# Optimization experiments

Measured on AMD Instinct MI355X. Metric: run time of the kernel, lower is better.

## Reference

```python
import jax, jax.numpy as jnp
import numpy as np

D_MODEL = 1024
H = 16
D_K = D_MODEL // H


def setup_inputs() -> dict:
    key = jax.random.key(0)
    ks = jax.random.split(key, 9)
    B, S = 4, 2048
    s = 1.0 / np.sqrt(D_MODEL)
    return {
        "query": jax.random.normal(ks[0], (B, S, D_MODEL), jnp.float32),
        "key_": jax.random.normal(ks[1], (B, S, D_MODEL), jnp.float32),
        "value": jax.random.normal(ks[2], (B, S, D_MODEL), jnp.float32),
        "Wq": jax.random.normal(ks[3], (D_MODEL, D_MODEL), jnp.float32) * s,
        "bq": jnp.zeros((D_MODEL,), jnp.float32),
        "Wk": jax.random.normal(ks[4], (D_MODEL, D_MODEL), jnp.float32) * s,
        "bk": jnp.zeros((D_MODEL,), jnp.float32),
        "Wv": jax.random.normal(ks[5], (D_MODEL, D_MODEL), jnp.float32) * s,
        "bv": jnp.zeros((D_MODEL,), jnp.float32),
    }


def reference(query, key_, value, Wq, bq, Wk, bk, Wv, bv):
    B, S, _ = query.shape
    # separate Q/K/V projections (torch Linear: x @ W.T + b)
    q = (query @ Wq.T + bq).reshape(B, S, H, D_K).transpose(0, 2, 1, 3)  # [B,H,S,Dk]
    k = (key_ @ Wk.T + bk).reshape(B, S, H, D_K).transpose(0, 2, 1, 3)
    v = (value @ Wv.T + bv).reshape(B, S, H, D_K).transpose(0, 2, 1, 3)
    # naive scaled dot-product attention (full [B,H,S,S] scores)
    scores = jnp.einsum("bhqd,bhkd->bhqk", q, k) / jnp.sqrt(jnp.float32(D_K))
    attn = jax.nn.softmax(scores, axis=-1)
    out = jnp.einsum("bhqk,bhkd->bhqd", attn, v)  # [B,H,S,Dk]
    # merge heads; NOTE: original forward never applies self.wo
    return out.transpose(0, 2, 1, 3).reshape(B, S, D_MODEL)
```

## Files before the change

kernel.cpp:

```cpp
#include <hip/hip_runtime.h>
#include <math.h>

#define DEVI __device__ __forceinline__

typedef short bf16x8 __attribute__((ext_vector_type(8)));
typedef float f32x4 __attribute__((ext_vector_type(4)));
typedef float f32x16 __attribute__((ext_vector_type(16)));
typedef unsigned short u16x8 __attribute__((ext_vector_type(8)));
typedef unsigned short u16x4 __attribute__((ext_vector_type(4)));
typedef unsigned int u32x2 __attribute__((ext_vector_type(2)));
typedef int i32x4 __attribute__((ext_vector_type(4)));

static constexpr int S_LEN = 2048;
static constexpr int DMODEL = 1024;
static constexpr int NH = 16;
static constexpr int DK = 64;

DEVI unsigned short f2bf(float f) {
  unsigned int u = __builtin_bit_cast(unsigned int, f);
  u = u + 0x7fffu + ((u >> 16) & 1u);
  return (unsigned short)(u >> 16);
}
DEVI unsigned cvtpk(float lo, float hi) {
  unsigned d;
  asm("v_cvt_pk_bf16_f32 %0, %1, %2" : "=v"(d) : "v"(lo), "v"(hi));
  return d;
}
DEVI float bitf(unsigned u) { return __builtin_bit_cast(float, u); }
DEVI unsigned bitu(float f) { return __builtin_bit_cast(unsigned, f); }

#if __has_builtin(__builtin_amdgcn_exp2f)
DEVI float fexp2(float x) { return __builtin_amdgcn_exp2f(x); }
#else
DEVI float fexp2(float x) { return __expf(x * 0.69314718055994531f); }
#endif

typedef __attribute__((address_space(3))) unsigned int lds_u32;
typedef __attribute__((address_space(1))) const unsigned int glb_u32;

DEVI void gload16(const void* g, void* lds) {
  __builtin_amdgcn_global_load_lds((glb_u32*)reinterpret_cast<uintptr_t>(g),
                                   (lds_u32*)reinterpret_cast<uintptr_t>(lds),
                                   16, 0, 0);
}

__global__ __launch_bounds__(256) void cvt_w3(const float* __restrict__ w0,
                                              const float* __restrict__ w1,
                                              const float* __restrict__ w2,
                                              unsigned short* __restrict__ out) {
  const int i = blockIdx.x * 256 + threadIdx.x;
  const int z = i >> 17, j = i & 131071;
  const float* in = (z == 0) ? w0 : (z == 1) ? w1 : w2;
  const float4* p = (const float4*)in + (size_t)j * 2;
  float4 a = p[0], b = p[1];
  u16x8 o;
  o[0] = f2bf(a.x); o[1] = f2bf(a.y); o[2] = f2bf(a.z); o[3] = f2bf(a.w);
  o[4] = f2bf(b.x); o[5] = f2bf(b.y); o[6] = f2bf(b.z); o[7] = f2bf(b.w);
  *((u16x8*)(out + (size_t)z * 1048576) + j) = o;
}

__global__ __launch_bounds__(256) void proj_all(const float* __restrict__ Aq,
                                                const float* __restrict__ Ak,
                                                const float* __restrict__ Av,
                                                const unsigned short* __restrict__ Wb,
                                                const float* __restrict__ bq,
                                                const float* __restrict__ bk,
                                                const float* __restrict__ bv,
                                                unsigned short* __restrict__ Qh,
                                                unsigned short* __restrict__ Kh,
                                                unsigned short* __restrict__ Vt,
                                                float qscale) {
  const int z = blockIdx.z;
  const float* A = (z == 0) ? Aq : (z == 1) ? Ak : Av;
  const unsigned short* W = Wb + (size_t)z * 1048576;
  const float* bias = (z == 0) ? bq : (z == 1) ? bk : bv;
  unsigned short* C = (z == 0) ? Qh : (z == 1) ? Kh : Vt;
  const float scale = (z == 0) ? qscale : 1.0f;
  const bool VT = (z == 2);

  __shared__ unsigned short As[2][128 * 32];
  __shared__ unsigned short Bs[2][128 * 32];
  const int m0 = blockIdx.x * 128, n0 = blockIdx.y * 128;
  const int tid = threadIdx.x, wid = tid >> 6, lane = tid & 63;
  const int l15 = lane & 15, lg = lane >> 4;
  const int mb = (wid >> 1) * 64, nb = (wid & 1) * 64;

  const int arow = wid * 32 + (lane >> 3);
  const int acolb = (lane & 7) * 16;

  f32x4 acc[4][4] = {};
  float4 a4[4];

  auto LOADA = [&](int kk) {
#pragma unroll
    for (int i = 0; i < 4; ++i)
      a4[i] = *(const float4*)((const char*)A + (size_t)(m0 + arow + i * 8) * 4096 +
                               kk * 128 + acolb);
  };
  auto GLOADW = [&](int b, int kk) {
#pragma unroll
    for (int i = 0; i < 2; ++i) {
      const int jb = (wid * 2 + i) * 1024;
      const int o = jb + lane * 16;
      gload16((const char*)W + (size_t)(n0 + (o >> 6)) * 2048 + kk * 64 + (o & 63),
              (char*)&Bs[b][0] + jb);
    }
  };
  auto WRITEA = [&](int b) {
#pragma unroll
    for (int i = 0; i < 4; ++i) {
      u32x2 wv;
      wv[0] = cvtpk(a4[i].x, a4[i].y);
      wv[1] = cvtpk(a4[i].z, a4[i].w);
      *(u32x2*)((char*)&As[b][0] + (arow + i * 8) * 64 + (lane & 7) * 8) = wv;
    }
  };

  LOADA(0);
  GLOADW(0, 0);
  asm volatile("s_waitcnt vmcnt(0)" ::: "memory");
  WRITEA(0);
  __syncthreads();

  int buf = 0;
  for (int kk = 0; kk < 32; ++kk) {
    if (kk < 31) {
      LOADA(kk + 1);
      GLOADW(buf ^ 1, kk + 1);
    }

    bf16x8 af[4], bfr[4];
#pragma unroll
    for (int ms = 0; ms < 4; ++ms)
      af[ms] = *(const bf16x8*)&As[buf][(mb + ms * 16 + l15) * 32 + lg * 8];
#pragma unroll
    for (int ns = 0; ns < 4; ++ns)
      bfr[ns] = *(const bf16x8*)&Bs[buf][(nb + ns * 16 + l15) * 32 + lg * 8];
#pragma unroll
    for (int ms = 0; ms < 4; ++ms)
#pragma unroll
      for (int ns = 0; ns < 4; ++ns)
        acc[ms][ns] = __builtin_amdgcn_mfma_f32_16x16x32_bf16(af[ms], bfr[ns],
                                                              acc[ms][ns], 0, 0, 0);

    if (kk < 31) {
      asm volatile("s_waitcnt vmcnt(0)" ::: "memory");
      WRITEA(buf ^ 1);
    }
    __syncthreads();
    buf ^= 1;
  }

#pragma unroll
  for (int ms = 0; ms < 4; ++ms) {
#pragma unroll
    for (int ns = 0; ns < 4; ++ns) {
      const int n = n0 + nb + ns * 16 + l15;
      const float bv = bias[n];
      const int mbase = m0 + mb + ms * 16 + lg * 4;
      if (VT) {
        u16x4 pk4;
#pragma unroll
        for (int r = 0; r < 4; ++r) pk4[r] = f2bf((acc[ms][ns][r] + bv) * scale);
        const size_t oi =
            (((size_t)(mbase >> 11) * NH + (n >> 6)) * DK + (n & 63)) * S_LEN + (mbase & 2047);
        *(u16x4*)&C[oi] = pk4;
      } else {
#pragma unroll
        for (int r = 0; r < 4; ++r) {
          const int m = mbase + r;
          const size_t oi =
              (((size_t)(m >> 11) * NH + (n >> 6)) * S_LEN + (m & 2047)) * DK + (n & 63);
          C[oi] = f2bf((acc[ms][ns][r] + bv) * scale);
        }
      }
    }
  }
}

__global__ __launch_bounds__(256) void attn_fwd(const unsigned short* __restrict__ Q,
                                                const unsigned short* __restrict__ K,
                                                const unsigned short* __restrict__ Vt,
                                                float* __restrict__ Out) {
  const int id = blockIdx.x;
  const int o = (id & 7) * 128 + (id >> 3);
  const int qt = o & 15, bh = o >> 4;

  const unsigned short* Qb = Q + (size_t)bh * S_LEN * DK;
  const char* Kb = (const char*)(K + (size_t)bh * S_LEN * DK);
  const char* Vb = (const char*)(Vt + (size_t)bh * DK * S_LEN);
  float* Ob = Out + (size_t)(bh >> 4) * S_LEN * DMODEL + (bh & 15) * DK;

  __shared__ unsigned short Ks[2][64][64];
  __shared__ unsigned short Vs[2][64][64];

  const int tid = threadIdx.x, w = tid >> 6, lane = tid & 63;
  const int l31 = lane & 31, hi = lane >> 5;
  const int q0 = qt * 128 + w * 32;
  const int swzr = (l31 & 7) ^ (((l31 >> 3) & 3) << 1);

  const int s8 = lane >> 3;
  int cs[2];
#pragma unroll
  for (int i = 0; i < 2; ++i)
    cs[i] = (((lane & 7) ^ s8) ^ (((w * 2 + i) & 3) << 1)) * 16;

  bf16x8 qf[4];
  {
    const unsigned short* qp = Qb + (size_t)(q0 + l31) * DK + hi * 8;
#pragma unroll
    for (int d = 0; d < 4; ++d) qf[d] = *(const bf16x8*)(qp + d * 16);
  }

  const i32x4 onesw = {0x3F803F80, 0x3F803F80, 0x3F803F80, 0x3F803F80};
  const bf16x8 ones = __builtin_bit_cast(bf16x8, onesw);

  f32x16 oacc0 = {}, oacc1 = {};
  f32x16 lsum = {};

  const int krow0 = w * 16;

#pragma unroll
  for (int i = 0; i < 2; ++i) {
    gload16(Kb + (size_t)(krow0 + i * 8 + s8) * 128 + cs[i],
            (char*)&Ks[0][krow0 + i * 8][0]);
    gload16(Vb + (size_t)(krow0 + i * 8 + s8) * 4096 + cs[i],
            (char*)&Vs[0][krow0 + i * 8][0]);
  }
  asm volatile("s_waitcnt vmcnt(0)" ::: "memory");
  __syncthreads();

  int buf = 0;
  for (int it = 0; it < 32; ++it) {
    if (it < 31) {
      const int j0 = (it + 1) * 64;
#pragma unroll
      for (int i = 0; i < 2; ++i) {
        gload16(Kb + (size_t)(j0 + krow0 + i * 8 + s8) * 128 + cs[i],
                (char*)&Ks[buf ^ 1][krow0 + i * 8][0]);
        gload16(Vb + (size_t)(krow0 + i * 8 + s8) * 4096 + j0 * 2 + cs[i],
                (char*)&Vs[buf ^ 1][krow0 + i * 8][0]);
      }
    }
    const char* ksb = (const char*)&Ks[buf][0][0];
    const char* vsb = (const char*)&Vs[buf][0][0];

    f32x16 sac0 = {}, sac1 = {};
#pragma unroll
    for (int d = 0; d < 4; ++d) {
      bf16x8 k0 = *(const bf16x8*)(ksb + (size_t)(l31)*128 + (((2 * d + hi) ^ swzr) * 16));
      bf16x8 k1 = *(const bf16x8*)(ksb + (size_t)(32 + l31) * 128 + (((2 * d + hi) ^ swzr) * 16));
      sac0 = __builtin_amdgcn_mfma_f32_32x32x16_bf16(k0, qf[d], sac0, 0, 0, 0);
      sac1 = __builtin_amdgcn_mfma_f32_32x32x16_bf16(k1, qf[d], sac1, 0, 0, 0);
    }

#pragma unroll
    for (int r = 0; r < 16; ++r) sac0[r] = fexp2(sac0[r]);
#pragma unroll
    for (int r = 0; r < 16; ++r) sac1[r] = fexp2(sac1[r]);

#pragma unroll
    for (int jb = 0; jb < 2; ++jb) {
      const f32x16& e = jb ? sac1 : sac0;
      unsigned pk[8];
#pragma unroll
      for (int m = 0; m < 8; ++m) pk[m] = cvtpk(e[2 * m], e[2 * m + 1]);
#pragma unroll
      for (int ks = 0; ks < 2; ++ks) {
        u32x2 s02 = __builtin_amdgcn_permlane32_swap(pk[4 * ks], pk[4 * ks + 2], false, false);
        u32x2 s13 = __builtin_amdgcn_permlane32_swap(pk[4 * ks + 1], pk[4 * ks + 3], false, false);
        i32x4 paw = {(int)s02[0], (int)s13[0], (int)s02[1], (int)s13[1]};
        bf16x8 pa = __builtin_bit_cast(bf16x8, paw);
        const int vslot = ((4 * jb + 2 * ks + hi) ^ swzr) * 16;
        bf16x8 v0 = *(const bf16x8*)(vsb + (size_t)(l31)*128 + vslot);
        bf16x8 v1 = *(const bf16x8*)(vsb + (size_t)(32 + l31) * 128 + vslot);
        oacc0 = __builtin_amdgcn_mfma_f32_32x32x16_bf16(pa, v0, oacc0, 0, 0, 0);
        oacc1 = __builtin_amdgcn_mfma_f32_32x32x16_bf16(pa, v1, oacc1, 0, 0, 0);
        lsum = __builtin_amdgcn_mfma_f32_32x32x16_bf16(pa, ones, lsum, 0, 0, 0);
      }
    }

    asm volatile("s_waitcnt vmcnt(0)" ::: "memory");
    __syncthreads();
    buf ^= 1;
  }

#pragma unroll
  for (int r = 0; r < 16; ++r) {
    const int cr = (r & 3) + 8 * (r >> 2);
    const float li = 1.f / lsum[r];
    const int qg = q0 + cr + 4 * hi;
    float* op = Ob + (size_t)qg * DMODEL;
    op[l31] = oacc0[r] * li;
    op[32 + l31] = oacc1[r] * li;
  }
}

extern "C" void kernel_launch(void* const* d_in, const int* in_sizes, int n_in,
                              void* d_out, int out_size, void* d_ws, size_t ws_size,
                              hipStream_t stream) {
  (void)in_sizes; (void)n_in; (void)out_size; (void)ws_size;
  const float* q_in = (const float*)d_in[0];
  const float* k_in = (const float*)d_in[1];
  const float* v_in = (const float*)d_in[2];
  const float* Wq = (const float*)d_in[3];
  const float* bq = (const float*)d_in[4];
  const float* Wk = (const float*)d_in[5];
  const float* bk = (const float*)d_in[6];
  const float* Wv = (const float*)d_in[7];
  const float* bv = (const float*)d_in[8];
  float* out = (float*)d_out;

  char* ws = (char*)d_ws;
  unsigned short* Wbf = (unsigned short*)(ws);
  unsigned short* Qh  = (unsigned short*)(ws + 6291456);
  unsigned short* Kh  = (unsigned short*)(ws + 23068672);
  unsigned short* Vt  = (unsigned short*)(ws + 39845888);

  const float qscale = 0.125f * 1.44269504088896340736f;

  cvt_w3<<<1536, 256, 0, stream>>>(Wq, Wk, Wv, Wbf);
  proj_all<<<dim3(64, 8, 3), 256, 0, stream>>>(q_in, k_in, v_in, Wbf,
                                               bq, bk, bv, Qh, Kh, Vt, qscale);
  attn_fwd<<<1024, 256, 0, stream>>>(Qh, Kh, Vt, out);
}
```

Baseline: 174.3 us.

## Deepen A-operand prefetch to two iterations in QKV projection GEMM

The fp32 A tile is now loaded two k-steps ahead into alternating register sets, so the global load has a full extra iteration of latency cover before it is converted and written to LDS. The full vmcnt(0) wait is replaced by a partial vmcnt(4) wait plus an explicit barrier and sched_barrier. This targets stalls where the projection GEMM waits on fp32 activation loads. In exchange it uses more registers (a second float4[4] set), which could lower occupancy, and the correctness of the partial wait depends on the order in which loads are issued.

```diff
diff --git a/kernel.cpp b/kernel.cpp
--- a/kernel.cpp
+++ b/kernel.cpp
@@ -89,9 +89,9 @@
   const int acolb = (lane & 7) * 16;
 
   f32x4 acc[4][4] = {};
-  float4 a4[4];
-
-  auto LOADA = [&](int kk) {
+  float4 a4A[4], a4B[4];
+
+  auto LOADA = [&](float4 (&a4)[4], int kk) {
 #pragma unroll
     for (int i = 0; i < 4; ++i)
       a4[i] = *(const float4*)((const char*)A + (size_t)(m0 + arow + i * 8) * 4096 +
@@ -106,7 +106,7 @@
               (char*)&Bs[b][0] + jb);
     }
   };
-  auto WRITEA = [&](int b) {
+  auto WRITEA = [&](int b, const float4 (&a4)[4]) {
 #pragma unroll
     for (int i = 0; i < 4; ++i) {
       u32x2 wv;
@@ -116,18 +116,10 @@
     }
   };
 
-  LOADA(0);
-  GLOADW(0, 0);
-  asm volatile("s_waitcnt vmcnt(0)" ::: "memory");
-  WRITEA(0);
-  __syncthreads();
-
   int buf = 0;
-  for (int kk = 0; kk < 32; ++kk) {
-    if (kk < 31) {
-      LOADA(kk + 1);
-      GLOADW(buf ^ 1, kk + 1);
-    }
+  auto ITER = [&](int kk, float4 (&cur)[4], float4 (&nxt)[4]) {
+    if (kk < 31) GLOADW(buf ^ 1, kk + 1);
+    if (kk < 30) LOADA(nxt, kk + 2);
 
     bf16x8 af[4], bfr[4];
 #pragma unroll
@@ -144,11 +136,28 @@
                                                               acc[ms][ns], 0, 0, 0);
 
     if (kk < 31) {
-      asm volatile("s_waitcnt vmcnt(0)" ::: "memory");
-      WRITEA(buf ^ 1);
-    }
-    __syncthreads();
+      WRITEA(buf ^ 1, cur);
+      if (kk < 30)
+        asm volatile("s_waitcnt vmcnt(4)" ::: "memory");
+      else
+        asm volatile("s_waitcnt vmcnt(0)" ::: "memory");
+      asm volatile("s_waitcnt lgkmcnt(0)" ::: "memory");
+      __builtin_amdgcn_s_barrier();
+      __builtin_amdgcn_sched_barrier(0);
+    }
     buf ^= 1;
+  };
+
+  LOADA(a4A, 0);
+  GLOADW(0, 0);
+  asm volatile("s_waitcnt vmcnt(0)" ::: "memory");
+  WRITEA(0, a4A);
+  __syncthreads();
+  LOADA(a4A, 1);
+
+  for (int k2 = 0; k2 < 16; ++k2) {
+    ITER(2 * k2, a4A, a4B);
+    ITER(2 * k2 + 1, a4B, a4A);
   }
 
 #pragma unroll
```

Measured after the change: 178.0 us. +2.1%, slower.
